# Kernel tuning notes

Measured on AMD Instinct MI355X. Metric: run time of the kernel, lower is better.

The kernel has to match this reference:

```python
import jax, jax.numpy as jnp
import numpy as np

N_GROUPS = 20   # hard-coded batch_size in NeRFGraph.forward
K = 3           # knn_graph k
IN_XYZ = 63
SKIP = 4
D = 8


def setup_inputs() -> dict:
    key = jax.random.key(0)
    B, W = 40960, 256
    G = B // N_GROUPS
    ks = jax.random.split(key, 22)

    def p(k, shape):
        fan_in = shape[-2] if len(shape) >= 2 else shape[-1]
        return jax.random.normal(k, shape, dtype=jnp.float32) / np.sqrt(fan_in)

    # batch assignment: exactly G nodes per group, randomly shuffled
    # (faithful to the np.zeros/fill/shuffle logic in the torch forward)
    batch_ids = jax.random.permutation(ks[1], jnp.repeat(jnp.arange(N_GROUPS, dtype=jnp.int32), G))

    return {
        "x": jax.random.normal(ks[0], (B, IN_XYZ + 27), dtype=jnp.float32),
        "batch_ids": batch_ids,
        "w0": p(ks[2], (IN_XYZ, W)), "b0": p(ks[3], (W,)),
        "w_mid": p(ks[4], (6, W, W)), "b_mid": p(ks[5], (6, W)),       # layers 1,2,3,5,6,7
        "w_skip": p(ks[6], (W + IN_XYZ, W)), "b_skip": p(ks[7], (W,)),  # layer 4 (skip)
        "w_final": p(ks[8], (W, W)), "b_final": p(ks[9], (W,)),
        "w_sigma": p(ks[10], (W, 1)), "b_sigma": p(ks[11], (1,)),
        "e1_w1": p(ks[12], (2 * (W + 27), W // 2)), "e1_b1": p(ks[13], (W // 2,)),
        "e1_w2": p(ks[14], (W // 2, W // 2)), "e1_b2": p(ks[15], (W // 2,)),
        "e2_w1": p(ks[16], (W, W // 2)), "e2_b1": p(ks[17], (W // 2,)),
        "e2_w2": p(ks[18], (W // 2, W // 2)), "e2_b2": p(ks[19], (W // 2,)),
        "w_rgb": p(ks[20], (W // 2, 3)), "b_rgb": p(ks[21], (3,)),
    }


def _knn(xyz, batch_ids):
    """k-NN within each of the N_GROUPS equal-size groups (loop=False).
    Returns (B, K) global neighbor indices for each node."""
    B = xyz.shape[0]
    G = B // N_GROUPS
    perm = jnp.argsort(batch_ids)                 # group nodes contiguously
    xg = xyz[perm].reshape(N_GROUPS, G, -1)
    sq = jnp.sum(xg * xg, axis=-1)                # (NG, G)
    d2 = sq[:, :, None] + sq[:, None, :] - 2.0 * jnp.einsum('gic,gjc->gij', xg, xg)
    d2 = jnp.where(jnp.eye(G, dtype=bool)[None], jnp.inf, d2)  # loop=False
    nbr_local = jax.lax.top_k(-d2, K)[1]          # (NG, G, K) local indices
    perm_g = perm.reshape(N_GROUPS, G)
    nbr_glob = jax.vmap(lambda p_, n_: p_[n_])(perm_g, nbr_local)  # (NG, G, K)
    inv = jnp.argsort(perm)
    return nbr_glob.reshape(B, K)[inv]


def _edge_conv(feat, nbr, w1, b1, w2, b2):
    # message: MLP(cat[x_i, x_j - x_i]); aggr='mean' over exactly K neighbors
    xi = feat[:, None, :]                         # (B, 1, C)
    xj = feat[nbr]                                # (B, K, C) gather
    tmp = jnp.concatenate([jnp.broadcast_to(xi, xj.shape), xj - xi], axis=-1)
    h = jax.nn.relu(tmp @ w1 + b1)
    h = jax.nn.relu(h @ w2 + b2)
    return h.mean(axis=1)                         # scatter-mean == mean over K


def reference(x, batch_ids, w0, b0, w_mid, b_mid, w_skip, b_skip, w_final, b_final,
              w_sigma, b_sigma, e1_w1, e1_b1, e1_w2, e1_b2, e2_w1, e2_b1, e2_w2, e2_b2,
              w_rgb, b_rgb):
    input_xyz, input_dir = x[:, :IN_XYZ], x[:, IN_XYZ:]
    nbr = _knn(input_xyz, batch_ids)
    h = jax.nn.relu(input_xyz @ w0 + b0)
    m = 0
    for i in range(1, D):
        if i == SKIP:
            h = jax.nn.relu(jnp.concatenate([input_xyz, h], axis=-1) @ w_skip + b_skip)
        else:
            h = jax.nn.relu(h @ w_mid[m] + b_mid[m])
            m += 1
    sigma = h @ w_sigma + b_sigma                  # (B, 1)
    feat = h @ w_final + b_final                   # xyz_encoding_final (no ReLU)
    d = _edge_conv(jnp.concatenate([feat, input_dir], axis=-1), nbr, e1_w1, e1_b1, e1_w2, e1_b2)
    d = _edge_conv(d, nbr, e2_w1, e2_b1, e2_w2, e2_b2)
    rgb = jax.nn.sigmoid(d @ w_rgb + b_rgb)        # (B, 3)
    return jnp.concatenate([rgb, sigma], axis=-1)  # (B, 4)
```

## Files before the change

### kernel.cpp

```cpp
#include <hip/hip_runtime.h>
#include <hip/hip_bf16.h>
#include <math.h>

#define B_TOTAL 40960
#define NGRP 20
#define GSZ 2048
#define CPART 4

typedef short short8 __attribute__((ext_vector_type(8)));
typedef float f32x4 __attribute__((ext_vector_type(4)));
typedef float f32x16 __attribute__((ext_vector_type(16)));
typedef _Float16 half8 __attribute__((ext_vector_type(8)));
typedef _Float16 half4 __attribute__((ext_vector_type(4)));

__device__ __forceinline__ unsigned short bf16rne(float v)
{
    unsigned int u = __float_as_uint(v);
    unsigned int r = (u + 0x7FFFu + ((u >> 16) & 1u)) >> 16;
    return (unsigned short)r;
}

__device__ __forceinline__ float bf2f(unsigned short h)
{
    return __uint_as_float((unsigned int)h << 16);
}

__device__ __forceinline__ void splitf16(const float* v, half8& hi, half8& lo)
{
    #pragma unroll
    for (int j = 0; j < 8; j++) {
        _Float16 h = (_Float16)v[j];
        hi[j] = h;
        lo[j] = (_Float16)(v[j] - (float)h);
    }
}

__device__ __forceinline__ unsigned int fkey(float f)
{
    unsigned int u = __float_as_uint(f);
    unsigned int m = (unsigned int)((int)u >> 31) | 0x80000000u;
    return u ^ m;
}

__device__ __forceinline__ void ins3p(unsigned int k, unsigned int i,
    unsigned int& k0, unsigned int& i0, unsigned int& k1, unsigned int& i1,
    unsigned int& k2, unsigned int& i2)
{
    bool c0 = k < k0;
    unsigned int tk = c0 ? k0 : k, ti = c0 ? i0 : i;
    k0 = c0 ? k : k0;  i0 = c0 ? i : i0;
    bool c1 = tk < k1;
    unsigned int sk = c1 ? k1 : tk, si = c1 ? i1 : ti;
    k1 = c1 ? tk : k1; i1 = c1 ? ti : i1;
    bool c2 = sk < k2;
    k2 = c2 ? sk : k2; i2 = c2 ? si : i2;
}

__device__ __forceinline__ void mergerow(unsigned int& k0, unsigned int& i0,
    unsigned int& k1, unsigned int& i1, unsigned int& k2, unsigned int& i2)
{
    #pragma unroll
    for (int m = 1; m <= 8; m <<= 1) {
        unsigned int ok0 = (unsigned int)__shfl_xor((int)k0, m);
        unsigned int oi0 = (unsigned int)__shfl_xor((int)i0, m);
        unsigned int ok1 = (unsigned int)__shfl_xor((int)k1, m);
        unsigned int oi1 = (unsigned int)__shfl_xor((int)i1, m);
        unsigned int ok2 = (unsigned int)__shfl_xor((int)k2, m);
        unsigned int oi2 = (unsigned int)__shfl_xor((int)i2, m);
        ins3p(ok0, oi0, k0, i0, k1, i1, k2, i2);
        ins3p(ok1, oi1, k0, i0, k1, i1, k2, i2);
        ins3p(ok2, oi2, k0, i0, k1, i1, k2, i2);
    }
}

__global__ __launch_bounds__(1024) void k_scatter_det(const int* __restrict__ bid,
                                                      int* __restrict__ grp)
{
    __shared__ int cnts[640];
    __shared__ int offs[640];
    const int tid = threadIdx.x;
    const int w = tid >> 6, lane = tid & 63;
    const int g = blockIdx.x;
    for (int c = 0; c < 40; c++) {
        int i = c * 1024 + tid;
        unsigned long long m = __ballot(bid[i] == g);
        if (lane == 0) cnts[c * 16 + w] = __popcll(m);
    }
    __syncthreads();
    if (w == 0) {
        int base = lane * 10;
        int loc[10];
        int s = 0;
        #pragma unroll
        for (int u = 0; u < 10; u++) { loc[u] = s; s += cnts[base + u]; }
        int incl = s;
        #pragma unroll
        for (int d = 1; d < 64; d <<= 1) {
            int t = __shfl_up(incl, d);
            if (lane >= d) incl += t;
        }
        int excl = incl - s;
        #pragma unroll
        for (int u = 0; u < 10; u++) offs[base + u] = excl + loc[u];
    }
    __syncthreads();
    for (int c = 0; c < 40; c++) {
        int i = c * 1024 + tid;
        bool f = (bid[i] == g);
        unsigned long long m = __ballot(f);
        unsigned long long below = m & ((lane == 63) ? 0x7FFFFFFFFFFFFFFFull
                                                     : ((1ull << lane) - 1ull));
        if (f) grp[g * GSZ + offs[c * 16 + w] + __popcll(below)] = i;
    }
}

__device__ __forceinline__ void do_wprep_trunk(int t, const float* __restrict__ w0,
    const float* __restrict__ wmid, const float* __restrict__ wskip,
    const float* __restrict__ wfin, _Float16* __restrict__ wfrag)
{
    const int CUMa[10] = {0,4,20,36,52,72,88,104,120,136};
    const int KCa[9]   = {4,16,16,16,20,16,16,16,16};
    int q = t >> 12;
    int L = 0;
    #pragma unroll
    for (int i = 0; i < 9; i++) if (q >= CUMa[i + 1]) L = i + 1;
    int cum = 0, kcn = 16;
    #pragma unroll
    for (int i = 0; i < 9; i++) if (L == i) { cum = CUMa[i]; kcn = KCa[i]; }
    int u = t - (cum << 12);
    int j = u & 7, lane = (u >> 3) & 63;
    int ckk = u >> 9;
    int kc = ckk % kcn, ct = ckk / kcn;
    int col = ct * 32 + (lane & 31);
    int k = kc * 16 + ((lane >> 5) << 3) + j;
    float w;
    if (L == 0)      w = (k < 63)  ? w0[k * 256 + col] : 0.f;
    else if (L == 4) w = (k < 256) ? wskip[(63 + k) * 256 + col]
                       : (k < 319) ? wskip[(k - 256) * 256 + col] : 0.f;
    else if (L == 8) w = wfin[k * 256 + col];
    else {
        int m = (L <= 3) ? (L - 1) : (L - 2);
        w = wmid[(size_t)m * 65536 + k * 256 + col];
    }
    wfrag[((size_t)cum << 12) + (size_t)ckk * 512 + lane * 8 + j] = (_Float16)w;
}

__device__ __forceinline__ void do_wprep_pq(int t, const float* __restrict__ src,
    int K, int KCN, _Float16* __restrict__ dst)
{
    int j = t & 7, lane = (t >> 3) & 63;
    int ckk = t >> 9;
    int kc = ckk % KCN, ct = ckk / KCN;
    int col = ct * 32 + (lane & 31);
    int k = kc * 16 + ((lane >> 5) << 3) + j;
    float w = 0.f;
    if (k < K) w = (col < 128) ? src[(size_t)k * 128 + col]
                               : src[(size_t)(K + k) * 128 + (col - 128)];
    dst[(size_t)ckk * 512 + lane * 8 + j] = (_Float16)w;
}

__device__ __forceinline__ void do_wprep_sq(int t, const float* __restrict__ src,
    _Float16* __restrict__ dst)
{
    int j = t & 7, lane = (t >> 3) & 63;
    int ckk = t >> 9;
    int kc = ckk & 7, ct = ckk >> 3;
    int col = ct * 32 + (lane & 31);
    int k = kc * 16 + ((lane >> 5) << 3) + j;
    dst[(size_t)ckk * 512 + lane * 8 + j] = (_Float16)src[(size_t)k * 128 + col];
}

__global__ void k_prep(const float* __restrict__ w0, const float* __restrict__ wmid,
                       const float* __restrict__ wskip, const float* __restrict__ wfin,
                       _Float16* __restrict__ wfrag,
                       const float* __restrict__ e1w1, _Float16* __restrict__ wfpq1,
                       const float* __restrict__ e2w1, _Float16* __restrict__ wfpq2,
                       const float* __restrict__ e1w2, _Float16* __restrict__ wfe1,
                       const float* __restrict__ e2w2, _Float16* __restrict__ wfe2)
{
    const int b = blockIdx.x;
    const int tid = threadIdx.x;
    if (b < 2176) {
        do_wprep_trunk(b * 256 + tid, w0, wmid, wskip, wfin, wfrag);
    } else if (b < 2464) {
        do_wprep_pq((b - 2176) * 256 + tid, e1w1, 283, 18, wfpq1);
    } else if (b < 2592) {
        do_wprep_pq((b - 2464) * 256 + tid, e2w1, 128, 8, wfpq2);
    } else if (b < 2656) {
        do_wprep_sq((b - 2592) * 256 + tid, e1w2, wfe1);
    } else {
        do_wprep_sq((b - 2656) * 256 + tid, e2w2, wfe2);
    }
}

__global__ __launch_bounds__(256) void k_gather(const float* __restrict__ x,
    const int* __restrict__ grp, unsigned short* __restrict__ xbh,
    unsigned short* __restrict__ xbl, float* __restrict__ cn)
{
    __shared__ float tile[128][65];
    __shared__ int ids[128];
    const int tid = threadIdx.x;
    const int g = blockIdx.y;
    const int q0 = blockIdx.x * 128;
    if (tid < 128) ids[tid] = grp[g * GSZ + q0 + tid];
    __syncthreads();
    for (int s = tid; s < 128 * 64; s += 256) {
        int q = s >> 6, d = s & 63;
        tile[q][d] = (d < 63) ? x[(size_t)ids[q] * 90 + d] : 0.f;
    }
    __syncthreads();
    if (tid < 128) {
        float a = 0.f;
        #pragma unroll
        for (int d = 0; d < 63; d++) a = fmaf(tile[tid][d], tile[tid][d], a);
        cn[g * GSZ + q0 + tid] = a;
    }
    for (int s = tid; s < 128 * 32; s += 256) {
        int q = s >> 5, dp = (s & 31) << 1;
        float v0 = tile[q][dp], v1 = tile[q][dp + 1];
        unsigned short h0 = bf16rne(v0), h1 = bf16rne(v1);
        unsigned short l0 = bf16rne(v0 - bf2f(h0)), l1 = bf16rne(v1 - bf2f(h1));
        size_t pt = (size_t)g * GSZ + q0 + q;
        ((unsigned int*)xbh)[pt * 32 + (dp >> 1)] = (unsigned int)h0 | ((unsigned int)h1 << 16);
        ((unsigned int*)xbl)[pt * 32 + (dp >> 1)] = (unsigned int)l0 | ((unsigned int)l1 << 16);
    }
}

template<int KCH, int KCX, int OUTMODE>
__device__ __forceinline__ void mlayer64(_Float16 (*Hh)[264], _Float16 (*Hl)[264],
    int rowbase, const float* __restrict__ x, const _Float16* __restrict__ wl,
    const float* __restrict__ bias, int lane, int wave)
{
    const int r31 = lane & 31, g = lane >> 5;
    constexpr int KC = KCH + KCX;
    const int ct = wave;
    f32x16 acc0, acc1;
    #pragma unroll
    for (int r = 0; r < 16; r++) { acc0[r] = 0.f; acc1[r] = 0.f; }
    const _Float16* wp = wl + (size_t)ct * KC * 512 + lane * 8;
    #pragma unroll
    for (int kc = 0; kc < KCH; kc++) {
        half8 ah0 = *(const half8*)&Hh[r31][kc * 16 + g * 8];
        half8 al0 = *(const half8*)&Hl[r31][kc * 16 + g * 8];
        half8 ah1 = *(const half8*)&Hh[32 + r31][kc * 16 + g * 8];
        half8 al1 = *(const half8*)&Hl[32 + r31][kc * 16 + g * 8];
        half8 b = *(const half8*)(wp + kc * 512);
        acc0 = __builtin_amdgcn_mfma_f32_32x32x16_f16(ah0, b, acc0, 0, 0, 0);
        acc1 = __builtin_amdgcn_mfma_f32_32x32x16_f16(ah1, b, acc1, 0, 0, 0);
        acc0 = __builtin_amdgcn_mfma_f32_32x32x16_f16(al0, b, acc0, 0, 0, 0);
        acc1 = __builtin_amdgcn_mfma_f32_32x32x16_f16(al1, b, acc1, 0, 0, 0);
    }
    #pragma unroll
    for (int t = 0; t < KCX; t++) {
        const int kc = KCH + t;
        float v0[8], v1[8];
        #pragma unroll
        for (int j = 0; j < 8; j++) {
            int kx = t * 16 + g * 8 + j;
            v0[j] = (kx < 63) ? x[(size_t)(rowbase + r31) * 90 + kx] : 0.f;
            v1[j] = (kx < 63) ? x[(size_t)(rowbase + 32 + r31) * 90 + kx] : 0.f;
        }
        half8 xh0, xl0, xh1, xl1;
        splitf16(v0, xh0, xl0);
        splitf16(v1, xh1, xl1);
        half8 b = *(const half8*)(wp + kc * 512);
        acc0 = __builtin_amdgcn_mfma_f32_32x32x16_f16(xh0, b, acc0, 0, 0, 0);
        acc1 = __builtin_amdgcn_mfma_f32_32x32x16_f16(xh1, b, acc1, 0, 0, 0);
        acc0 = __builtin_amdgcn_mfma_f32_32x32x16_f16(xl0, b, acc0, 0, 0, 0);
        acc1 = __builtin_amdgcn_mfma_f32_32x32x16_f16(xl1, b, acc1, 0, 0, 0);
    }
    const float bv = bias[ct * 32 + r31];
    __syncthreads();
    #pragma unroll
    for (int r = 0; r < 16; r++) {
        int row = (r & 3) + 8 * (r >> 2) + 4 * g;
        float v0 = acc0[r] + bv;
        float v1 = acc1[r] + bv;
        if (OUTMODE == 0) { v0 = fmaxf(v0, 0.f); v1 = fmaxf(v1, 0.f); }
        _Float16 h0 = (_Float16)v0, h1 = (_Float16)v1;
        Hh[row][ct * 32 + r31] = h0;
        Hl[row][ct * 32 + r31] = (_Float16)(v0 - (float)h0);
        Hh[32 + row][ct * 32 + r31] = h1;
        Hl[32 + row][ct * 32 + r31] = (_Float16)(v1 - (float)h1);
    }
    __syncthreads();
}

__global__ __launch_bounds__(512, 4) void k_main(const float* __restrict__ x,
    const _Float16* __restrict__ wfrag,
    const float* __restrict__ b0, const float* __restrict__ bmid,
    const float* __restrict__ bskip, const float* __restrict__ bfin,
    const float* __restrict__ wsig, const float* __restrict__ bsig,
    const _Float16* __restrict__ wfpq1, float* __restrict__ PQ,
    float* __restrict__ out,
    const unsigned short* __restrict__ xbh, const unsigned short* __restrict__ xbl,
    const float* __restrict__ cn, unsigned long long* __restrict__ pkey)
{
    __shared__ union SM {
        struct { _Float16 Hh[64][264]; _Float16 Hl[64][264];
                 _Float16 Dh[64][40];  _Float16 Dl[64][40]; } t;
        char knn[2][16384];
    } sm;
    const int tid = threadIdx.x;
    const int lane = tid & 63;
    const int wave = tid >> 6;
    const int r31 = lane & 31, g = lane >> 5;

    if (blockIdx.x < 640) {
        const int rowbase = blockIdx.x * 64;
        _Float16 (*Hh)[264] = sm.t.Hh;
        _Float16 (*Hl)[264] = sm.t.Hl;
        for (int s = tid; s < 64 * 32; s += 512) {
            int r = s >> 5, d = s & 31;
            float v = (d < 27) ? x[(size_t)(rowbase + r) * 90 + 63 + d] : 0.f;
            _Float16 h = (_Float16)v;
            sm.t.Dh[r][d] = h;
            sm.t.Dl[r][d] = (_Float16)(v - (float)h);
        }
        const _Float16* W = wfrag;
        mlayer64<0, 4, 0>(Hh, Hl, rowbase, x, W + (size_t)0   * 4096, b0,          lane, wave);
        mlayer64<16,0, 0>(Hh, Hl, rowbase, x, W + (size_t)4   * 4096, bmid + 0,    lane, wave);
        mlayer64<16,0, 0>(Hh, Hl, rowbase, x, W + (size_t)20  * 4096, bmid + 256,  lane, wave);
        mlayer64<16,0, 0>(Hh, Hl, rowbase, x, W + (size_t)36  * 4096, bmid + 512,  lane, wave);
        mlayer64<16,4, 0>(Hh, Hl, rowbase, x, W + (size_t)52  * 4096, bskip,       lane, wave);
        mlayer64<16,0, 0>(Hh, Hl, rowbase, x, W + (size_t)72  * 4096, bmid + 768,  lane, wave);
        mlayer64<16,0, 0>(Hh, Hl, rowbase, x, W + (size_t)88  * 4096, bmid + 1024, lane, wave);
        mlayer64<16,0, 0>(Hh, Hl, rowbase, x, W + (size_t)104 * 4096, bmid + 1280, lane, wave);
        if (wave < 2) {
            const int row = wave * 32 + r31;
            float s = 0.f;
            #pragma unroll
            for (int kk = 0; kk < 32; kk++) {
                half4 hh = *(const half4*)&Hh[row][g * 128 + kk * 4];
                half4 hl = *(const half4*)&Hl[row][g * 128 + kk * 4];
                float4 wv = *(const float4*)&wsig[g * 128 + kk * 4];
                s = fmaf((float)hh[0] + (float)hl[0], wv.x, s);
                s = fmaf((float)hh[1] + (float)hl[1], wv.y, s);
                s = fmaf((float)hh[2] + (float)hl[2], wv.z, s);
                s = fmaf((float)hh[3] + (float)hl[3], wv.w, s);
            }
            s += __shfl_xor(s, 32);
            if (lane < 32) out[(size_t)(rowbase + row) * 4 + 3] = s + bsig[0];
        }
        mlayer64<16,0, 2>(Hh, Hl, rowbase, x, W + (size_t)120 * 4096, bfin, lane, wave);
        {
            const int ct = wave;
            f32x16 p0, p1;
            #pragma unroll
            for (int r = 0; r < 16; r++) { p0[r] = 0.f; p1[r] = 0.f; }
            const _Float16* wp = wfpq1 + (size_t)ct * 18 * 512 + lane * 8;
            #pragma unroll
            for (int kc = 0; kc < 16; kc++) {
                half8 ah0 = *(const half8*)&Hh[r31][kc * 16 + g * 8];
                half8 al0 = *(const half8*)&Hl[r31][kc * 16 + g * 8];
                half8 ah1 = *(const half8*)&Hh[32 + r31][kc * 16 + g * 8];
                half8 al1 = *(const half8*)&Hl[32 + r31][kc * 16 + g * 8];
                half8 b = *(const half8*)(wp + kc * 512);
                p0 = __builtin_amdgcn_mfma_f32_32x32x16_f16(ah0, b, p0, 0, 0, 0);
                p1 = __builtin_amdgcn_mfma_f32_32x32x16_f16(ah1, b, p1, 0, 0, 0);
                p0 = __builtin_amdgcn_mfma_f32_32x32x16_f16(al0, b, p0, 0, 0, 0);
                p1 = __builtin_amdgcn_mfma_f32_32x32x16_f16(al1, b, p1, 0, 0, 0);
            }
            #pragma unroll
            for (int kc = 16; kc < 18; kc++) {
                const int dc = (kc - 16) * 16 + g * 8;
                half8 ah0 = *(const half8*)&sm.t.Dh[r31][dc];
                half8 al0 = *(const half8*)&sm.t.Dl[r31][dc];
                half8 ah1 = *(const half8*)&sm.t.Dh[32 + r31][dc];
                half8 al1 = *(const half8*)&sm.t.Dl[32 + r31][dc];
                half8 b = *(const half8*)(wp + kc * 512);
                p0 = __builtin_amdgcn_mfma_f32_32x32x16_f16(ah0, b, p0, 0, 0, 0);
                p1 = __builtin_amdgcn_mfma_f32_32x32x16_f16(ah1, b, p1, 0, 0, 0);
                p0 = __builtin_amdgcn_mfma_f32_32x32x16_f16(al0, b, p0, 0, 0, 0);
                p1 = __builtin_amdgcn_mfma_f32_32x32x16_f16(al1, b, p1, 0, 0, 0);
            }
            #pragma unroll
            for (int r = 0; r < 16; r++) {
                int row = (r & 3) + 8 * (r >> 2) + 4 * g;
                PQ[(size_t)(rowbase + row) * 256 + ct * 32 + r31] = p0[r];
                PQ[(size_t)(rowbase + 32 + row) * 256 + ct * 32 + r31] = p1[r];
            }
        }
    } else {
        const int bb = blockIdx.x - 640;
        const int gg = bb >> 6;
        const int rem = bb & 63;
        const int part = rem >> 4;
        const int qx = rem & 15;
        const int qt0 = qx * 128 + wave * 16;
        const size_t gbase = (size_t)gg * GSZ;
        const int lp = lane & 15;
        const int kgrp = lane >> 4;
        const int kg = kgrp << 3;
        char (*cbuf)[16384] = sm.knn;

        const size_t qb = (gbase + qt0 + lp) * 64;
        short8 ah0 = *(const short8*)(xbh + qb + kg);
        short8 ah1 = *(const short8*)(xbh + qb + 32 + kg);
        short8 al0 = *(const short8*)(xbl + qb + kg);
        short8 al1 = *(const short8*)(xbl + qb + 32 + kg);

        const int qp0 = qt0 + (kgrp << 2);

        unsigned int K00 = ~0u, I00 = 0, K01 = ~0u, I01 = 0, K02 = ~0u, I02 = 0;
        unsigned int K10 = ~0u, I10 = 0, K11 = ~0u, I11 = 0, K12 = ~0u, I12 = 0;
        unsigned int K20 = ~0u, I20 = 0, K21 = ~0u, I21 = 0, K22 = ~0u, I22 = 0;
        unsigned int K30 = ~0u, I30 = 0, K31 = ~0u, I31 = 0, K32 = ~0u, I32 = 0;

        const int cbeg = part * (GSZ / CPART);

        short8 st0, st1;
        {
            size_t cb = (gbase + cbeg + lane) * 64;
            st0 = *(const short8*)(xbh + cb + wave * 8);
            st1 = *(const short8*)(xbl + cb + wave * 8);
        }
        *(short8*)&cbuf[0][(wave << 10) + (lane << 4)] = st0;
        *(short8*)&cbuf[0][((8 + wave) << 10) + (lane << 4)] = st1;

        for (int ch = 0; ch < 8; ch++) {
            const int cur = ch & 1;
            __syncthreads();
            if (ch < 7) {
                size_t cb = (gbase + cbeg + (ch + 1) * 64 + lane) * 64;
                st0 = *(const short8*)(xbh + cb + wave * 8);
                st1 = *(const short8*)(xbl + cb + wave * 8);
            }
            const int cc0 = cbeg + ch * 64;
            #pragma unroll
            for (int ct = 0; ct < 4; ct++) {
                const int coff = ((ct * 16 + lp) << 4);
                short8 bh0 = *(const short8*)&cbuf[cur][((kgrp)      << 10) + coff];
                short8 bh1 = *(const short8*)&cbuf[cur][((4 + kgrp)  << 10) + coff];
                short8 bl0 = *(const short8*)&cbuf[cur][((8 + kgrp)  << 10) + coff];
                short8 bl1 = *(const short8*)&cbuf[cur][((12 + kgrp) << 10) + coff];
                f32x4 acc = {0.f, 0.f, 0.f, 0.f};
                acc = __builtin_amdgcn_mfma_f32_16x16x32_bf16(ah0, bh0, acc, 0, 0, 0);
                acc = __builtin_amdgcn_mfma_f32_16x16x32_bf16(ah1, bh1, acc, 0, 0, 0);
                acc = __builtin_amdgcn_mfma_f32_16x16x32_bf16(al0, bh0, acc, 0, 0, 0);
                acc = __builtin_amdgcn_mfma_f32_16x16x32_bf16(al1, bh1, acc, 0, 0, 0);
                acc = __builtin_amdgcn_mfma_f32_16x16x32_bf16(ah0, bl0, acc, 0, 0, 0);
                acc = __builtin_amdgcn_mfma_f32_16x16x32_bf16(ah1, bl1, acc, 0, 0, 0);
                const float cnv = cn[gbase + cc0 + ct * 16 + lp];
                const int cpos = cc0 + ct * 16 + lp;
                const unsigned int ci = (unsigned int)cpos;
                {
                    unsigned int k = fkey(fmaf(-2.f, acc[0], cnv));
                    k = (cpos == qp0 + 0) ? 0xFFFFFFFFu : k;
                    ins3p(k, ci, K00, I00, K01, I01, K02, I02);
                }
                {
                    unsigned int k = fkey(fmaf(-2.f, acc[1], cnv));
                    k = (cpos == qp0 + 1) ? 0xFFFFFFFFu : k;
                    ins3p(k, ci, K10, I10, K11, I11, K12, I12);
                }
                {
                    unsigned int k = fkey(fmaf(-2.f, acc[2], cnv));
                    k = (cpos == qp0 + 2) ? 0xFFFFFFFFu : k;
                    ins3p(k, ci, K20, I20, K21, I21, K22, I22);
                }
                {
                    unsigned int k = fkey(fmaf(-2.f, acc[3], cnv));
                    k = (cpos == qp0 + 3) ? 0xFFFFFFFFu : k;
                    ins3p(k, ci, K30, I30, K31, I31, K32, I32);
                }
            }
            if (ch < 7) {
                *(short8*)&cbuf[cur ^ 1][(wave << 10) + (lane << 4)] = st0;
                *(short8*)&cbuf[cur ^ 1][((8 + wave) << 10) + (lane << 4)] = st1;
            }
        }

        mergerow(K00, I00, K01, I01, K02, I02);
        mergerow(K10, I10, K11, I11, K12, I12);
        mergerow(K20, I20, K21, I21, K22, I22);
        mergerow(K30, I30, K31, I31, K32, I32);

        if (lp == 0) {
            size_t ob = (gbase + (size_t)qp0) * (CPART * 3) + part * 3;
            pkey[ob + 0]  = ((unsigned long long)K00 << 32) | I00;
            pkey[ob + 1]  = ((unsigned long long)K01 << 32) | I01;
            pkey[ob + 2]  = ((unsigned long long)K02 << 32) | I02;
            pkey[ob + 12] = ((unsigned long long)K10 << 32) | I10;
            pkey[ob + 13] = ((unsigned long long)K11 << 32) | I11;
            pkey[ob + 14] = ((unsigned long long)K12 << 32) | I12;
            pkey[ob + 24] = ((unsigned long long)K20 << 32) | I20;
            pkey[ob + 25] = ((unsigned long long)K21 << 32) | I21;
            pkey[ob + 26] = ((unsigned long long)K22 << 32) | I22;
            pkey[ob + 36] = ((unsigned long long)K30 << 32) | I30;
            pkey[ob + 37] = ((unsigned long long)K31 << 32) | I31;
            pkey[ob + 38] = ((unsigned long long)K32 << 32) | I32;
        }
    }
}

__device__ __forceinline__ void ins3u(unsigned long long k,
    unsigned long long& k0, unsigned long long& k1, unsigned long long& k2)
{
    if (k < k0)      { k2 = k1; k1 = k0; k0 = k; }
    else if (k < k1) { k2 = k1; k1 = k; }
    else if (k < k2) { k2 = k; }
}

__global__ void k_knn_merge(const unsigned long long* __restrict__ pkey,
                            const int* __restrict__ grp, int* __restrict__ nbr)
{
    int t = blockIdx.x * 256 + threadIdx.x;
    if (t >= NGRP * GSZ) return;
    int g = t >> 11;
    unsigned long long k0 = ~0ull, k1 = ~0ull, k2 = ~0ull;
    const unsigned long long* pk = pkey + (size_t)t * (CPART * 3);
    #pragma unroll
    for (int r = 0; r < CPART * 3; r++) ins3u(pk[r], k0, k1, k2);
    int qi = grp[t];
    nbr[(size_t)qi * 3 + 0] = grp[(g << 11) + (int)(k0 & 0xFFFFFFFFull)];
    nbr[(size_t)qi * 3 + 1] = grp[(g << 11) + (int)(k1 & 0xFFFFFFFFull)];
    nbr[(size_t)qi * 3 + 2] = grp[(g << 11) + (int)(k2 & 0xFFFFFFFFull)];
}

template<int RGB>
__global__ __launch_bounds__(256) void k_edge_mfma(const float* __restrict__ PQ,
    const float* __restrict__ b1, const _Float16* __restrict__ wf2,
    const float* __restrict__ b2, const int* __restrict__ nbr,
    const _Float16* __restrict__ wfpq2, float* __restrict__ pqout,
    const float* __restrict__ wrgb, const float* __restrict__ brgb,
    float* __restrict__ out)
{
    __shared__ _Float16 Hh[128][136];
    __shared__ _Float16 Hl[128][136];
    const int tid = threadIdx.x;
    const int lane = tid & 63, wave = tid >> 6;
    const int r31 = lane & 31, g = lane >> 5;
    const int n0 = blockIdx.x * 32;

    for (int s = tid; s < 128 * 32; s += 256) {
        int e = s >> 5, c4 = (s & 31) << 2;
        int n = e >> 2, jj = e & 3;
        half4 zh = {(_Float16)0.f, (_Float16)0.f, (_Float16)0.f, (_Float16)0.f};
        if (jj < 3) {
            int i = n0 + n;
            int j = nbr[(size_t)i * 3 + jj];
            float4 p  = *(const float4*)&PQ[(size_t)i * 256 + c4];
            float4 qi = *(const float4*)&PQ[(size_t)i * 256 + 128 + c4];
            float4 qj = *(const float4*)&PQ[(size_t)j * 256 + 128 + c4];
            float4 bv = *(const float4*)&b1[c4];
            float v[4];
            v[0] = fmaxf(p.x + bv.x + qj.x - qi.x, 0.f);
            v[1] = fmaxf(p.y + bv.y + qj.y - qi.y, 0.f);
            v[2] = fmaxf(p.z + bv.z + qj.z - qi.z, 0.f);
            v[3] = fmaxf(p.w + bv.w + qj.w - qi.w, 0.f);
            half4 hh, hl;
            #pragma unroll
            for (int u = 0; u < 4; u++) {
                _Float16 h = (_Float16)v[u];
                hh[u] = h;
                hl[u] = (_Float16)(v[u] - (float)h);
            }
            *(half4*)&Hh[e][c4] = hh;
            *(half4*)&Hl[e][c4] = hl;
        } else {
            *(half4*)&Hh[e][c4] = zh;
            *(half4*)&Hl[e][c4] = zh;
        }
    }
    __syncthreads();

    const int ct = wave;
    f32x16 a0, a1, a2, a3;
    #pragma unroll
    for (int r = 0; r < 16; r++) { a0[r] = 0.f; a1[r] = 0.f; a2[r] = 0.f; a3[r] = 0.f; }
    const _Float16* wp = wf2 + (size_t)ct * 8 * 512 + lane * 8;
    #pragma unroll
    for (int kc = 0; kc < 8; kc++) {
        half8 b = *(const half8*)(wp + kc * 512);
        half8 h0 = *(const half8*)&Hh[r31][kc * 16 + g * 8];
        half8 l0 = *(const half8*)&Hl[r31][kc * 16 + g * 8];
        a0 = __builtin_amdgcn_mfma_f32_32x32x16_f16(h0, b, a0, 0, 0, 0);
        a0 = __builtin_amdgcn_mfma_f32_32x32x16_f16(l0, b, a0, 0, 0, 0);
        half8 h1 = *(const half8*)&Hh[32 + r31][kc * 16 + g * 8];
        half8 l1 = *(const half8*)&Hl[32 + r31][kc * 16 + g * 8];
        a1 = __builtin_amdgcn_mfma_f32_32x32x16_f16(h1, b, a1, 0, 0, 0);
        a1 = __builtin_amdgcn_mfma_f32_32x32x16_f16(l1, b, a1, 0, 0, 0);
        half8 h2 = *(const half8*)&Hh[64 + r31][kc * 16 + g * 8];
        half8 l2 = *(const half8*)&Hl[64 + r31][kc * 16 + g * 8];
        a2 = __builtin_amdgcn_mfma_f32_32x32x16_f16(h2, b, a2, 0, 0, 0);
        a2 = __builtin_amdgcn_mfma_f32_32x32x16_f16(l2, b, a2, 0, 0, 0);
        half8 h3 = *(const half8*)&Hh[96 + r31][kc * 16 + g * 8];
        half8 l3 = *(const half8*)&Hl[96 + r31][kc * 16 + g * 8];
        a3 = __builtin_amdgcn_mfma_f32_32x32x16_f16(h3, b, a3, 0, 0, 0);
        a3 = __builtin_amdgcn_mfma_f32_32x32x16_f16(l3, b, a3, 0, 0, 0);
    }
    const float bv = b2[ct * 32 + r31];
    const int col = ct * 32 + r31;

    if (!RGB) {
        __syncthreads();
        #pragma unroll
        for (int q = 0; q < 4; q++) {
            float s0 = fmaxf(a0[4*q] + bv, 0.f) + fmaxf(a0[4*q+1] + bv, 0.f) + fmaxf(a0[4*q+2] + bv, 0.f);
            float s1 = fmaxf(a1[4*q] + bv, 0.f) + fmaxf(a1[4*q+1] + bv, 0.f) + fmaxf(a1[4*q+2] + bv, 0.f);
            float s2 = fmaxf(a2[4*q] + bv, 0.f) + fmaxf(a2[4*q+1] + bv, 0.f) + fmaxf(a2[4*q+2] + bv, 0.f);
            float s3 = fmaxf(a3[4*q] + bv, 0.f) + fmaxf(a3[4*q+1] + bv, 0.f) + fmaxf(a3[4*q+2] + bv, 0.f);
            int nq = 2 * q + g;
            float v0 = s0 * (1.f / 3.f), v1 = s1 * (1.f / 3.f);
            float v2 = s2 * (1.f / 3.f), v3 = s3 * (1.f / 3.f);
            _Float16 h0 = (_Float16)v0, h1 = (_Float16)v1, h2 = (_Float16)v2, h3 = (_Float16)v3;
            Hh[0  + nq][col] = h0; Hl[0  + nq][col] = (_Float16)(v0 - (float)h0);
            Hh[8  + nq][col] = h1; Hl[8  + nq][col] = (_Float16)(v1 - (float)h1);
            Hh[16 + nq][col] = h2; Hl[16 + nq][col] = (_Float16)(v2 - (float)h2);
            Hh[24 + nq][col] = h3; Hl[24 + nq][col] = (_Float16)(v3 - (float)h3);
        }
        __syncthreads();
        const int ct0 = wave * 2;
        f32x16 p0, p1;
        #pragma unroll
        for (int r = 0; r < 16; r++) { p0[r] = 0.f; p1[r] = 0.f; }
        const _Float16* wq0 = wfpq2 + (size_t)ct0 * 8 * 512 + lane * 8;
        const _Float16* wq1 = wq0 + (size_t)8 * 512;
        #pragma unroll
        for (int kc = 0; kc < 8; kc++) {
            half8 ah = *(const half8*)&Hh[r31][kc * 16 + g * 8];
            half8 al = *(const half8*)&Hl[r31][kc * 16 + g * 8];
            half8 b0v = *(const half8*)(wq0 + kc * 512);
            half8 b1v = *(const half8*)(wq1 + kc * 512);
            p0 = __builtin_amdgcn_mfma_f32_32x32x16_f16(ah, b0v, p0, 0, 0, 0);
            p1 = __builtin_amdgcn_mfma_f32_32x32x16_f16(ah, b1v, p1, 0, 0, 0);
            p0 = __builtin_amdgcn_mfma_f32_32x32x16_f16(al, b0v, p0, 0, 0, 0);
            p1 = __builtin_amdgcn_mfma_f32_32x32x16_f16(al, b1v, p1, 0, 0, 0);
        }
        #pragma unroll
        for (int r = 0; r < 16; r++) {
            int row = (r & 3) + 8 * (r >> 2) + 4 * g;
            pqout[(size_t)(n0 + row) * 256 + ct0 * 32 + r31] = p0[r];
            pqout[(size_t)(n0 + row) * 256 + ct0 * 32 + 32 + r31] = p1[r];
        }
    } else {
        __syncthreads();
        float* d2L = (float*)&Hh[0][0];
        #pragma unroll
        for (int q = 0; q < 4; q++) {
            float s0 = fmaxf(a0[4*q] + bv, 0.f) + fmaxf(a0[4*q+1] + bv, 0.f) + fmaxf(a0[4*q+2] + bv, 0.f);
            float s1 = fmaxf(a1[4*q] + bv, 0.f) + fmaxf(a1[4*q+1] + bv, 0.f) + fmaxf(a1[4*q+2] + bv, 0.f);
            float s2 = fmaxf(a2[4*q] + bv, 0.f) + fmaxf(a2[4*q+1] + bv, 0.f) + fmaxf(a2[4*q+2] + bv, 0.f);
            float s3 = fmaxf(a3[4*q] + bv, 0.f) + fmaxf(a3[4*q+1] + bv, 0.f) + fmaxf(a3[4*q+2] + bv, 0.f);
            int nq = 2 * q + g;
            d2L[(0  + nq) * 132 + col] = s0 * (1.f / 3.f);
            d2L[(8  + nq) * 132 + col] = s1 * (1.f / 3.f);
            d2L[(16 + nq) * 132 + col] = s2 * (1.f / 3.f);
            d2L[(24 + nq) * 132 + col] = s3 * (1.f / 3.f);
        }
        __syncthreads();
        if (tid < 96) {
            int n = tid / 3, ch = tid - 3 * (tid / 3);
            float s = brgb[ch];
            for (int k = 0; k < 128; k++) s = fmaf(d2L[n * 132 + k], wrgb[k * 3 + ch], s);
            out[(size_t)(n0 + n) * 4 + ch] = 1.f / (1.f + expf(-s));
        }
    }
}

extern "C" void kernel_launch(void* const* d_in, const int* in_sizes, int n_in,
                              void* d_out, int out_size, void* d_ws, size_t ws_size,
                              hipStream_t stream)
{
    const float* x     = (const float*)d_in[0];
    const int*   bid   = (const int*)d_in[1];
    const float* w0    = (const float*)d_in[2];
    const float* b0    = (const float*)d_in[3];
    const float* wmid  = (const float*)d_in[4];
    const float* bmid  = (const float*)d_in[5];
    const float* wskip = (const float*)d_in[6];
    const float* bskip = (const float*)d_in[7];
    const float* wfin  = (const float*)d_in[8];
    const float* bfin  = (const float*)d_in[9];
    const float* wsig  = (const float*)d_in[10];
    const float* bsig  = (const float*)d_in[11];
    const float* e1w1  = (const float*)d_in[12];
    const float* e1b1  = (const float*)d_in[13];
    const float* e1w2  = (const float*)d_in[14];
    const float* e1b2  = (const float*)d_in[15];
    const float* e2w1  = (const float*)d_in[16];
    const float* e2b1  = (const float*)d_in[17];
    const float* e2w2  = (const float*)d_in[18];
    const float* e2b2  = (const float*)d_in[19];
    const float* wrgb  = (const float*)d_in[20];
    const float* brgb  = (const float*)d_in[21];
    float* out = (float*)d_out;

    char* ws = (char*)d_ws;
    int* grp = (int*)(ws + 256);
    int* nbr = (int*)(ws + 164096);
    _Float16* wfpq1 = (_Float16*)(ws + 655616);
    _Float16* wfpq2 = (_Float16*)(ws + 950528);
    _Float16* wfe1  = (_Float16*)(ws + 1081600);
    _Float16* wfe2  = (_Float16*)(ws + 1147136);
    float* bufA = (float*)(ws + (2 << 20));
    float* bufB = bufA + (size_t)B_TOTAL * 256;

    unsigned short* xbh = (unsigned short*)bufA;
    unsigned short* xbl = xbh + (size_t)B_TOTAL * 64;
    float* cn   = (float*)(xbl + (size_t)B_TOTAL * 64);
    unsigned long long* pkey = (unsigned long long*)(cn + B_TOTAL);
    _Float16* wfrag = (_Float16*)((char*)bufA + ((size_t)20 << 20));
    float* PQ  = bufB;
    float* PQ2 = bufA;

    k_prep<<<2720, 256, 0, stream>>>(w0, wmid, wskip, wfin, wfrag,
                                     e1w1, wfpq1, e2w1, wfpq2, e1w2, wfe1, e2w2, wfe2);
    k_scatter_det<<<NGRP, 1024, 0, stream>>>(bid, grp);
    k_gather<<<dim3(GSZ / 128, NGRP), 256, 0, stream>>>(x, grp, xbh, xbl, cn);
    k_main<<<640 + 1280, 512, 0, stream>>>(x, wfrag, b0, bmid, bskip, bfin,
                                           wsig, bsig, wfpq1, PQ, out,
                                           xbh, xbl, cn, pkey);
    k_knn_merge<<<(NGRP * GSZ + 255) / 256, 256, 0, stream>>>(pkey, grp, nbr);
    k_edge_mfma<0><<<B_TOTAL / 32, 256, 0, stream>>>(PQ, e1b1, wfe1, e1b2, nbr,
                                                     wfpq2, PQ2, nullptr, nullptr, nullptr);
    k_edge_mfma<1><<<B_TOTAL / 32, 256, 0, stream>>>(PQ2, e2b1, wfe2, e2b2, nbr,
                                                     nullptr, nullptr, wrgb, brgb, out);
}
```

Baseline: 321.1 us.

## Fuse weight prep, group scatter, and xyz gather into one front kernel

Merges the weight-fragment preparation, the deterministic per-group scatter and the xyz gather/bf16-split into a single launch of 700 blocks of 1024 threads. Blocks 0-19 each handle one whole group, scattering its ids into shared memory and then gathering in 8 passes of 256 rows. The remaining blocks do the weight conversion in parallel. This removes two kernel launches and the grp round-trip between them, but the gather is now serialized inside only 20 blocks instead of spread across 320, which may lengthen the critical path.

```diff
diff --git a/kernel.cpp b/kernel.cpp
--- a/kernel.cpp
+++ b/kernel.cpp
@@ -70,47 +70,6 @@
         ins3p(ok0, oi0, k0, i0, k1, i1, k2, i2);
         ins3p(ok1, oi1, k0, i0, k1, i1, k2, i2);
         ins3p(ok2, oi2, k0, i0, k1, i1, k2, i2);
-    }
-}
-
-__global__ __launch_bounds__(1024) void k_scatter_det(const int* __restrict__ bid,
-                                                      int* __restrict__ grp)
-{
-    __shared__ int cnts[640];
-    __shared__ int offs[640];
-    const int tid = threadIdx.x;
-    const int w = tid >> 6, lane = tid & 63;
-    const int g = blockIdx.x;
-    for (int c = 0; c < 40; c++) {
-        int i = c * 1024 + tid;
-        unsigned long long m = __ballot(bid[i] == g);
-        if (lane == 0) cnts[c * 16 + w] = __popcll(m);
-    }
-    __syncthreads();
-    if (w == 0) {
-        int base = lane * 10;
-        int loc[10];
-        int s = 0;
-        #pragma unroll
-        for (int u = 0; u < 10; u++) { loc[u] = s; s += cnts[base + u]; }
-        int incl = s;
-        #pragma unroll
-        for (int d = 1; d < 64; d <<= 1) {
-            int t = __shfl_up(incl, d);
-            if (lane >= d) incl += t;
-        }
-        int excl = incl - s;
-        #pragma unroll
-        for (int u = 0; u < 10; u++) offs[base + u] = excl + loc[u];
-    }
-    __syncthreads();
-    for (int c = 0; c < 40; c++) {
-        int i = c * 1024 + tid;
-        bool f = (bid[i] == g);
-        unsigned long long m = __ballot(f);
-        unsigned long long below = m & ((lane == 63) ? 0x7FFFFFFFFFFFFFFFull
-                                                     : ((1ull << lane) - 1ull));
-        if (f) grp[g * GSZ + offs[c * 16 + w] + __popcll(below)] = i;
     }
 }
 
@@ -170,59 +129,103 @@
     dst[(size_t)ckk * 512 + lane * 8 + j] = (_Float16)src[(size_t)k * 128 + col];
 }
 
-__global__ void k_prep(const float* __restrict__ w0, const float* __restrict__ wmid,
-                       const float* __restrict__ wskip, const float* __restrict__ wfin,
-                       _Float16* __restrict__ wfrag,
-                       const float* __restrict__ e1w1, _Float16* __restrict__ wfpq1,
-                       const float* __restrict__ e2w1, _Float16* __restrict__ wfpq2,
-                       const float* __restrict__ e1w2, _Float16* __restrict__ wfe1,
-                       const float* __restrict__ e2w2, _Float16* __restrict__ wfe2)
-{
+__global__ __launch_bounds__(1024) void k_front(const int* __restrict__ bid,
+    int* __restrict__ grp, const float* __restrict__ x,
+    unsigned short* __restrict__ xbh, unsigned short* __restrict__ xbl,
+    float* __restrict__ cn,
+    const float* __restrict__ w0, const float* __restrict__ wmid,
+    const float* __restrict__ wskip, const float* __restrict__ wfin,
+    _Float16* __restrict__ wfrag,
+    const float* __restrict__ e1w1, _Float16* __restrict__ wfpq1,
+    const float* __restrict__ e2w1, _Float16* __restrict__ wfpq2,
+    const float* __restrict__ e1w2, _Float16* __restrict__ wfe1,
+    const float* __restrict__ e2w2, _Float16* __restrict__ wfe2)
+{
+    __shared__ int cnts[640];
+    __shared__ int offs[640];
+    __shared__ int ids[GSZ];
+    __shared__ float tile[256][65];
+    const int tid = threadIdx.x;
     const int b = blockIdx.x;
-    const int tid = threadIdx.x;
-    if (b < 2176) {
-        do_wprep_trunk(b * 256 + tid, w0, wmid, wskip, wfin, wfrag);
-    } else if (b < 2464) {
-        do_wprep_pq((b - 2176) * 256 + tid, e1w1, 283, 18, wfpq1);
-    } else if (b < 2592) {
-        do_wprep_pq((b - 2464) * 256 + tid, e2w1, 128, 8, wfpq2);
-    } else if (b < 2656) {
-        do_wprep_sq((b - 2592) * 256 + tid, e1w2, wfe1);
-    } else {
-        do_wprep_sq((b - 2656) * 256 + tid, e2w2, wfe2);
-    }
-}
-
-__global__ __launch_bounds__(256) void k_gather(const float* __restrict__ x,
-    const int* __restrict__ grp, unsigned short* __restrict__ xbh,
-    unsigned short* __restrict__ xbl, float* __restrict__ cn)
-{
-    __shared__ float tile[128][65];
-    __shared__ int ids[128];
-    const int tid = threadIdx.x;
-    const int g = blockIdx.y;
-    const int q0 = blockIdx.x * 128;
-    if (tid < 128) ids[tid] = grp[g * GSZ + q0 + tid];
+
+    if (b >= 20) {
+        const int b2 = b - 20;
+        if (b2 < 544) {
+            do_wprep_trunk(b2 * 1024 + tid, w0, wmid, wskip, wfin, wfrag);
+        } else if (b2 < 616) {
+            do_wprep_pq((b2 - 544) * 1024 + tid, e1w1, 283, 18, wfpq1);
+        } else if (b2 < 648) {
+            do_wprep_pq((b2 - 616) * 1024 + tid, e2w1, 128, 8, wfpq2);
+        } else if (b2 < 664) {
+            do_wprep_sq((b2 - 648) * 1024 + tid, e1w2, wfe1);
+        } else {
+            do_wprep_sq((b2 - 664) * 1024 + tid, e2w2, wfe2);
+        }
+        return;
+    }
+
+    const int w = tid >> 6, lane = tid & 63;
+    const int g = b;
+    for (int c = 0; c < 40; c++) {
+        int i = c * 1024 + tid;
+        unsigned long long m = __ballot(bid[i] == g);
+        if (lane == 0) cnts[c * 16 + w] = __popcll(m);
+    }
     __syncthreads();
-    for (int s = tid; s < 128 * 64; s += 256) {
-        int q = s >> 6, d = s & 63;
-        tile[q][d] = (d < 63) ? x[(size_t)ids[q] * 90 + d] : 0.f;
+    if (w == 0) {
+        int base = lane * 10;
+        int loc[10];
+        int s = 0;
+        #pragma unroll
+        for (int u = 0; u < 10; u++) { loc[u] = s; s += cnts[base + u]; }
+        int incl = s;
+        #pragma unroll
+        for (int d = 1; d < 64; d <<= 1) {
+            int t = __shfl_up(incl, d);
+            if (lane >= d) incl += t;
+        }
+        int excl = incl - s;
+        #pragma unroll
+        for (int u = 0; u < 10; u++) offs[base + u] = excl + loc[u];
     }
     __syncthreads();
-    if (tid < 128) {
-        float a = 0.f;
-        #pragma unroll
-        for (int d = 0; d < 63; d++) a = fmaf(tile[tid][d], tile[tid][d], a);
-        cn[g * GSZ + q0 + tid] = a;
-    }
-    for (int s = tid; s < 128 * 32; s += 256) {
-        int q = s >> 5, dp = (s & 31) << 1;
-        float v0 = tile[q][dp], v1 = tile[q][dp + 1];
-        unsigned short h0 = bf16rne(v0), h1 = bf16rne(v1);
-        unsigned short l0 = bf16rne(v0 - bf2f(h0)), l1 = bf16rne(v1 - bf2f(h1));
-        size_t pt = (size_t)g * GSZ + q0 + q;
-        ((unsigned int*)xbh)[pt * 32 + (dp >> 1)] = (unsigned int)h0 | ((unsigned int)h1 << 16);
-        ((unsigned int*)xbl)[pt * 32 + (dp >> 1)] = (unsigned int)l0 | ((unsigned int)l1 << 16);
+    for (int c = 0; c < 40; c++) {
+        int i = c * 1024 + tid;
+        bool f = (bid[i] == g);
+        unsigned long long m = __ballot(f);
+        unsigned long long below = m & ((lane == 63) ? 0x7FFFFFFFFFFFFFFFull
+                                                     : ((1ull << lane) - 1ull));
+        if (f) {
+            int pos = offs[c * 16 + w] + __popcll(below);
+            grp[g * GSZ + pos] = i;
+            ids[pos] = i;
+        }
+    }
+    __syncthreads();
+
+    for (int pass = 0; pass < 8; pass++) {
+        const int q0 = pass * 256;
+        for (int s = tid; s < 256 * 64; s += 1024) {
+            int q = s >> 6, d = s & 63;
+            tile[q][d] = (d < 63) ? x[(size_t)ids[q0 + q] * 90 + d] : 0.f;
+        }
+        __syncthreads();
+        if (tid < 256) {
+            float a = 0.f;
+            #pragma unroll
+            for (int d = 0; d < 63; d++) a = fmaf(tile[tid][d], tile[tid][d], a);
+            cn[g * GSZ + q0 + tid] = a;
+        }
+        for (int s = tid; s < 256 * 32; s += 1024) {
+            int q = s >> 5, dp = (s & 31) << 1;
+            float v0 = tile[q][dp], v1 = tile[q][dp + 1];
+            unsigned short h0 = bf16rne(v0), h1 = bf16rne(v1);
+            unsigned short l0 = bf16rne(v0 - bf2f(h0)), l1 = bf16rne(v1 - bf2f(h1));
+            size_t pt = (size_t)g * GSZ + q0 + q;
+            ((unsigned int*)xbh)[pt * 32 + (dp >> 1)] = (unsigned int)h0 | ((unsigned int)h1 << 16);
+            ((unsigned int*)xbl)[pt * 32 + (dp >> 1)] = (unsigned int)l0 | ((unsigned int)l1 << 16);
+        }
+        __syncthreads();
     }
 }
 
@@ -705,10 +708,10 @@
     float* PQ  = bufB;
     float* PQ2 = bufA;
 
-    k_prep<<<2720, 256, 0, stream>>>(w0, wmid, wskip, wfin, wfrag,
-                                     e1w1, wfpq1, e2w1, wfpq2, e1w2, wfe1, e2w2, wfe2);
-    k_scatter_det<<<NGRP, 1024, 0, stream>>>(bid, grp);
-    k_gather<<<dim3(GSZ / 128, NGRP), 256, 0, stream>>>(x, grp, xbh, xbl, cn);
+    k_front<<<700, 1024, 0, stream>>>(bid, grp, x, xbh, xbl, cn,
+                                      w0, wmid, wskip, wfin, wfrag,
+                                      e1w1, wfpq1, e2w1, wfpq2,
+                                      e1w2, wfe1, e2w2, wfe2);
     k_main<<<640 + 1280, 512, 0, stream>>>(x, wfrag, b0, bmid, bskip, bfin,
                                            wsig, bsig, wfpq1, PQ, out,
                                            xbh, xbl, cn, pkey);
```

After: 357.6 us. 1.11x slower.
